# Kernel optimization log

Measured on AMD Instinct MI355X. Metric: run time of the kernel, lower is better.

## Reference

```python
import jax, jax.numpy as jnp
import numpy as np

N_HEADS = 8
EMBED_DIM = 512
HEAD_DIM = EMBED_DIM // N_HEADS
INPUT_DIM = 512


def setup_inputs() -> dict:
    key = jax.random.key(0)
    ks = jax.random.split(key, 9)
    B, N = 4, 2048
    s_in = 1.0 / np.sqrt(INPUT_DIM)
    s_e = 1.0 / np.sqrt(EMBED_DIM)
    return {
        "q": jax.random.normal(ks[0], (B, N, INPUT_DIM), dtype=jnp.float32),
        "wq": jax.random.uniform(ks[1], (EMBED_DIM, INPUT_DIM), jnp.float32, -s_in, s_in),
        "bq": jax.random.uniform(ks[2], (EMBED_DIM,), jnp.float32, -s_in, s_in),
        "wk": jax.random.uniform(ks[3], (EMBED_DIM, INPUT_DIM), jnp.float32, -s_in, s_in),
        "bk": jax.random.uniform(ks[4], (EMBED_DIM,), jnp.float32, -s_in, s_in),
        "wv": jax.random.uniform(ks[5], (EMBED_DIM, INPUT_DIM), jnp.float32, -s_in, s_in),
        "bv": jax.random.uniform(ks[6], (EMBED_DIM,), jnp.float32, -s_in, s_in),
        "wo": jax.random.uniform(ks[7], (EMBED_DIM, EMBED_DIM), jnp.float32, -s_e, s_e),
        "bo": jax.random.uniform(ks[8], (EMBED_DIM,), jnp.float32, -s_e, s_e),
    }


def reference(q, wq, bq, wk, bk, wv, bv, wo, bo):
    B, N, _ = q.shape
    # linear projections (torch Linear: x @ W.T + b)
    Q = (q @ wq.T + bq).reshape(B, N, N_HEADS, HEAD_DIM).transpose(0, 2, 1, 3)
    K = (q @ wk.T + bk).reshape(B, N, N_HEADS, HEAD_DIM).transpose(0, 2, 1, 3)
    V = (q @ wv.T + bv).reshape(B, N, N_HEADS, HEAD_DIM).transpose(0, 2, 1, 3)
    scores = jnp.einsum("bhqd,bhkd->bhqk", Q, K) / jnp.sqrt(
        jnp.asarray(HEAD_DIM, dtype=q.dtype)
    )
    weights = jax.nn.softmax(scores, axis=-1)
    out = jnp.einsum("bhqk,bhkd->bhqd", weights, V)  # [B,H,N,Dh]
    out = out.transpose(0, 2, 1, 3).reshape(B, N, EMBED_DIM)
    return out @ wo.T + bo
```

## Files before the change

### kernel.cpp

```cpp
#include <hip/hip_runtime.h>
#include <hip/hip_bf16.h>
#include <math.h>

#define SEQ    2048
#define DH     64
#define EMB    512
#define INDIM  512
#define NHEADS 8
#define BATCH  4
#define MTOT   (BATCH * SEQ)

typedef __attribute__((ext_vector_type(8))) short bf16x8;
typedef __attribute__((ext_vector_type(4))) float f32x4;

__device__ __forceinline__ ushort f2bf(float x) {
  union { float f; unsigned u; } v; v.f = x;
  unsigned r = v.u + 0x7FFFu + ((v.u >> 16) & 1u);
  return (ushort)(r >> 16);
}

__device__ __forceinline__ unsigned cvt_pk_bf16(float lo, float hi) {
  unsigned r;
  asm("v_cvt_pk_bf16_f32 %0, %1, %2" : "=v"(r) : "v"(lo), "v"(hi));
  return r;
}

__device__ __forceinline__ float fast_exp2(float x) {
  float r;
  asm("v_exp_f32 %0, %1" : "=v"(r) : "v"(x));
  return r;
}

__device__ __forceinline__ void permswap32(unsigned &x, unsigned &y) {
  asm("v_permlane32_swap_b32 %0, %1" : "+v"(x), "+v"(y));
}

__global__ __launch_bounds__(256) void conv_bf16(const float* __restrict__ src,
                                                 ushort* __restrict__ dst, int n8) {
  const int i = blockIdx.x * 256 + threadIdx.x;
  if (i >= n8) return;
  const float4 a = ((const float4*)src)[i * 2];
  const float4 b = ((const float4*)src)[i * 2 + 1];
  uint4 o;
  o.x = cvt_pk_bf16(a.x, a.y);
  o.y = cvt_pk_bf16(a.z, a.w);
  o.z = cvt_pk_bf16(b.x, b.y);
  o.w = cvt_pk_bf16(b.z, b.w);
  ((uint4*)dst)[i] = o;
}

__global__ __launch_bounds__(256) void conv_bf16_w4(
    const float* __restrict__ w0, const float* __restrict__ w1,
    const float* __restrict__ w2, const float* __restrict__ w3,
    ushort* __restrict__ dst, int n8per) {
  const int i = blockIdx.x * 256 + threadIdx.x;
  if (i >= n8per) return;
  const float* src = (blockIdx.y == 0) ? w0 : (blockIdx.y == 1) ? w1
                   : (blockIdx.y == 2) ? w2 : w3;
  ushort* d = dst + (size_t)blockIdx.y * n8per * 8;
  const float4 a = ((const float4*)src)[i * 2];
  const float4 b = ((const float4*)src)[i * 2 + 1];
  uint4 o;
  o.x = cvt_pk_bf16(a.x, a.y);
  o.y = cvt_pk_bf16(a.z, a.w);
  o.z = cvt_pk_bf16(b.x, b.y);
  o.w = cvt_pk_bf16(b.z, b.w);
  ((uint4*)d)[i] = o;
}

template <int MODE>
__global__ __launch_bounds__(256) void mfma_gemm(
    const ushort* __restrict__ A, const ushort* __restrict__ W,
    const float* __restrict__ b0, const float* __restrict__ b1,
    const float* __restrict__ b2,
    ushort* __restrict__ outQ, ushort* __restrict__ outK,
    ushort* __restrict__ outVT, float* __restrict__ outF) {
  __shared__ __align__(16) char smem[MODE == 0 ? 35840 : 16384];
  ushort* As = (ushort*)smem;
  ushort* Bs = (ushort*)(smem + 8192);
  ushort* Tl = (ushort*)smem;
  ushort* Tl2 = (ushort*)smem;

  const int bm = blockIdx.x * 128;
  const int bn = blockIdx.y * 128;
  const int tid = threadIdx.x;
  const int wave = tid >> 6, lane = tid & 63;
  const int g = lane >> 4, ln = lane & 15;
  const int wr = wave >> 1, wc = wave & 1;

  f32x4 acc[4][4];
#pragma unroll
  for (int m = 0; m < 4; ++m)
#pragma unroll
    for (int n = 0; n < 4; ++n) acc[m][n] = (f32x4){0.f, 0.f, 0.f, 0.f};

  const size_t a_base = (size_t)(bm + wave * 16 + (lane >> 2)) * INDIM + (lane & 3) * 8;
  const size_t b_base = (size_t)(bn + wave * 16 + (lane >> 2)) * INDIM + (lane & 3) * 8;
  ushort* ldsA0 = As + wave * 512;
  ushort* ldsA1 = As + 2048 + wave * 512;
  ushort* ldsB0 = Bs + wave * 512;
  ushort* ldsB1 = Bs + 2048 + wave * 512;

  for (int k0 = 0; k0 < INDIM; k0 += 32) {
    __syncthreads();
    __builtin_amdgcn_global_load_lds(
        (const __attribute__((address_space(1))) void*)(A + a_base + k0),
        (__attribute__((address_space(3))) void*)ldsA0, 16, 0, 0);
    __builtin_amdgcn_global_load_lds(
        (const __attribute__((address_space(1))) void*)(A + a_base + 64 * INDIM + k0),
        (__attribute__((address_space(3))) void*)ldsA1, 16, 0, 0);
    __builtin_amdgcn_global_load_lds(
        (const __attribute__((address_space(1))) void*)(W + b_base + k0),
        (__attribute__((address_space(3))) void*)ldsB0, 16, 0, 0);
    __builtin_amdgcn_global_load_lds(
        (const __attribute__((address_space(1))) void*)(W + b_base + 64 * INDIM + k0),
        (__attribute__((address_space(3))) void*)ldsB1, 16, 0, 0);
    __syncthreads();

    bf16x8 af[4], bfv[4];
#pragma unroll
    for (int m = 0; m < 4; ++m)
      af[m] = *(const bf16x8*)&As[(64 * wr + 16 * m + ln) * 32 + 8 * g];
#pragma unroll
    for (int n = 0; n < 4; ++n)
      bfv[n] = *(const bf16x8*)&Bs[(64 * wc + 16 * n + ln) * 32 + 8 * g];
#pragma unroll
    for (int m = 0; m < 4; ++m)
#pragma unroll
      for (int n = 0; n < 4; ++n)
        acc[m][n] = __builtin_amdgcn_mfma_f32_16x16x32_bf16(af[m], bfv[n], acc[m][n], 0, 0, 0);
  }

  if (MODE == 1) {
#pragma unroll
    for (int n = 0; n < 4; ++n) {
      const int e = bn + 64 * wc + 16 * n + ln;
      const float bv = b0[e];
#pragma unroll
      for (int m = 0; m < 4; ++m)
#pragma unroll
        for (int r = 0; r < 4; ++r) {
          const int row = bm + 64 * wr + 16 * m + 4 * g + r;
          outF[(size_t)row * EMB + e] = acc[m][n][r] + bv;
        }
    }
    return;
  }

  const int which = bn >> 9;
  const float* bias = (which == 0) ? b0 : (which == 1) ? b1 : b2;

  if (which < 2) {
    const float scl = (which == 0) ? 0.18033688f : 1.0f;
    ushort* dst = (which == 0) ? outQ : outK;
    __syncthreads();
#pragma unroll
    for (int n = 0; n < 4; ++n) {
      const int cl = 64 * wc + 16 * n + ln;
      const float bv = bias[(bn & 511) + cl];
#pragma unroll
      for (int m = 0; m < 4; ++m)
#pragma unroll
        for (int r = 0; r < 4; ++r) {
          const int rl = 64 * wr + 16 * m + 4 * g + r;
          Tl2[rl * 136 + cl] = f2bf((acc[m][n][r] + bv) * scl);
        }
    }
    __syncthreads();
#pragma unroll
    for (int j = 0; j < 8; ++j) {
      const int cid = j * 256 + tid;
      const int seg = cid >> 3;
      const int l8 = cid & 7;
      const int rl = seg >> 1, half = seg & 1;
      const int row = bm + rl;
      const int b = row >> 11, nn = row & (SEQ - 1);
      const int h = ((bn & 511) >> 6) + half;
      const bf16x8 v = *(const bf16x8*)&Tl2[rl * 136 + half * 64 + l8 * 8];
      *(bf16x8*)&dst[(((size_t)(b * NHEADS + h) * SEQ) + nn) * DH + l8 * 8] = v;
    }
  } else {
    __syncthreads();
#pragma unroll
    for (int n = 0; n < 4; ++n) {
      const int cl = 64 * wc + 16 * n + ln;
      const float bv = bias[(bn & 511) + cl];
#pragma unroll
      for (int m = 0; m < 4; ++m)
#pragma unroll
        for (int r = 0; r < 4; ++r) {
          const int rl = 64 * wr + 16 * m + 4 * g + r;
          Tl[cl * 140 + rl] = f2bf(acc[m][n][r] + bv);
        }
    }
    __syncthreads();
    const int c = tid >> 1;
    const int rh = (tid & 1) * 64;
    const int e = (bn & 511) + c;
    const int h = e >> 6, d = e & 63;
    const int b = bm >> 11;
    const int nn0 = (bm & (SEQ - 1)) + rh;
    ushort* drow = outVT + (((size_t)(b * NHEADS + h) * DH) + d) * SEQ + nn0;
#pragma unroll
    for (int j = 0; j < 8; ++j)
      *(bf16x8*)&drow[j * 8] = *(const bf16x8*)&Tl[c * 140 + rh + j * 8];
  }
}

__global__ __launch_bounds__(256, 4) void attn_mfma(const ushort* __restrict__ Q,
                                                    const ushort* __restrict__ K,
                                                    const ushort* __restrict__ VT,
                                                    ushort* __restrict__ O) {
  __shared__ __align__(16) ushort Kl[2][64 * 72];
  __shared__ __align__(16) ushort Vl[2][64 * 72];

  const int tid = threadIdx.x;
  const int wave = tid >> 6, lane = tid & 63;
  const int g = lane >> 4, ln = lane & 15;

  const int orig = blockIdx.x;
  const int swz = (orig & 7) * 128 + (orig >> 3);
  const int bh = swz >> 5;
  const int qx = swz & 31;
  const int qbase = qx * 64 + wave * 16;

  const ushort* Qb = Q + ((size_t)bh * SEQ + qbase) * DH;
  const ushort* Kb = K + (size_t)bh * SEQ * DH;
  const ushort* Vb = VT + (size_t)bh * DH * SEQ;

  const bf16x8 qf0 = *(const bf16x8*)&Qb[ln * DH + 8 * g];
  const bf16x8 qf1 = *(const bf16x8*)&Qb[ln * DH + 32 + 8 * g];

  bf16x8 vones;
#pragma unroll
  for (int i = 0; i < 8; ++i) vones[i] = (short)0x3F80;

  f32x4 oacc[4];
  f32x4 oaccD = (f32x4){0.f, 0.f, 0.f, 0.f};
#pragma unroll
  for (int t = 0; t < 4; ++t) oacc[t] = (f32x4){0.f, 0.f, 0.f, 0.f};

  const int skv = tid >> 3, sd = (tid & 7) * 8;
  const int dt = tid >> 2, kc = (tid & 3) * 8;
  const int pr0 = skv ^ (((((skv >> 2) ^ (skv >> 3)) & 1)) * 12);
  const int s32 = skv + 32;
  const int pr1 = s32 ^ (((((s32 >> 2) ^ (s32 >> 3)) & 1)) * 12);

  bf16x8 k0v = *(const bf16x8*)&Kb[(size_t)skv * DH + sd];
  bf16x8 k1v = *(const bf16x8*)&Kb[(size_t)(32 + skv) * DH + sd];
  bf16x8 v0v = *(const bf16x8*)&Vb[(size_t)dt * SEQ + kc];
  bf16x8 v1v = *(const bf16x8*)&Vb[(size_t)dt * SEQ + 32 + kc];
  *(bf16x8*)&Kl[0][pr0 * 72 + sd] = k0v;
  *(bf16x8*)&Kl[0][pr1 * 72 + sd] = k1v;
  *(bf16x8*)&Vl[0][dt * 72 + kc] = v0v;
  *(bf16x8*)&Vl[0][dt * 72 + 32 + kc] = v1v;
  k0v = *(const bf16x8*)&Kb[(size_t)(64 + skv) * DH + sd];
  k1v = *(const bf16x8*)&Kb[(size_t)(96 + skv) * DH + sd];
  v0v = *(const bf16x8*)&Vb[(size_t)dt * SEQ + 64 + kc];
  v1v = *(const bf16x8*)&Vb[(size_t)dt * SEQ + 96 + kc];
  asm volatile("s_waitcnt lgkmcnt(0)" ::: "memory");
  __builtin_amdgcn_s_barrier();

  for (int it = 0; it < 32; ++it) {
    const int cur = it & 1;
    ushort* Kc = Kl[cur];
    ushort* Vc = Vl[cur];

    if (it < 31) {
      ushort* Kn = Kl[cur ^ 1];
      ushort* Vn = Vl[cur ^ 1];
      *(bf16x8*)&Kn[pr0 * 72 + sd] = k0v;
      *(bf16x8*)&Kn[pr1 * 72 + sd] = k1v;
      *(bf16x8*)&Vn[dt * 72 + kc] = v0v;
      *(bf16x8*)&Vn[dt * 72 + 32 + kc] = v1v;
    }
    {
      const int nxt = (it + 2 < 32) ? (it + 2) * 64 : 31 * 64;
      k0v = *(const bf16x8*)&Kb[(size_t)(nxt + skv) * DH + sd];
      k1v = *(const bf16x8*)&Kb[(size_t)(nxt + 32 + skv) * DH + sd];
      v0v = *(const bf16x8*)&Vb[(size_t)dt * SEQ + nxt + kc];
      v1v = *(const bf16x8*)&Vb[(size_t)dt * SEQ + nxt + 32 + kc];
    }

    bf16x8 ka[4][2], vb[2][4];
#pragma unroll
    for (int t = 0; t < 4; ++t) {
      ka[t][0] = *(const bf16x8*)&Kc[(16 * t + ln) * 72 + 8 * g];
      ka[t][1] = *(const bf16x8*)&Kc[(16 * t + ln) * 72 + 32 + 8 * g];
    }
#pragma unroll
    for (int c = 0; c < 2; ++c)
#pragma unroll
      for (int t = 0; t < 4; ++t)
        vb[c][t] = *(const bf16x8*)&Vc[(16 * t + ln) * 72 + 32 * c + 8 * g];

    f32x4 s0 = (f32x4){0.f, 0.f, 0.f, 0.f};
    f32x4 s1 = s0, s2 = s0, s3 = s0;
    __builtin_amdgcn_s_setprio(1);
    s0 = __builtin_amdgcn_mfma_f32_16x16x32_bf16(ka[0][0], qf0, s0, 0, 0, 0);
    s1 = __builtin_amdgcn_mfma_f32_16x16x32_bf16(ka[1][0], qf0, s1, 0, 0, 0);
    s2 = __builtin_amdgcn_mfma_f32_16x16x32_bf16(ka[2][0], qf0, s2, 0, 0, 0);
    s3 = __builtin_amdgcn_mfma_f32_16x16x32_bf16(ka[3][0], qf0, s3, 0, 0, 0);
    s0 = __builtin_amdgcn_mfma_f32_16x16x32_bf16(ka[0][1], qf1, s0, 0, 0, 0);
    s1 = __builtin_amdgcn_mfma_f32_16x16x32_bf16(ka[1][1], qf1, s1, 0, 0, 0);
    s2 = __builtin_amdgcn_mfma_f32_16x16x32_bf16(ka[2][1], qf1, s2, 0, 0, 0);
    s3 = __builtin_amdgcn_mfma_f32_16x16x32_bf16(ka[3][1], qf1, s3, 0, 0, 0);
    __builtin_amdgcn_s_setprio(0);

    float p0[4], p1[4], p2[4], p3[4];
#pragma unroll
    for (int r = 0; r < 4; ++r) {
      p0[r] = fast_exp2(s0[r]);
      p1[r] = fast_exp2(s1[r]);
      p2[r] = fast_exp2(s2[r]);
      p3[r] = fast_exp2(s3[r]);
    }

    unsigned a0 = cvt_pk_bf16(p0[0], p0[1]);
    unsigned a2 = cvt_pk_bf16(p1[0], p1[1]);
    unsigned a1 = cvt_pk_bf16(p0[2], p0[3]);
    unsigned a3 = cvt_pk_bf16(p1[2], p1[3]);
    permswap32(a0, a2);
    permswap32(a1, a3);
    unsigned b0 = cvt_pk_bf16(p2[0], p2[1]);
    unsigned b2 = cvt_pk_bf16(p3[0], p3[1]);
    unsigned b1 = cvt_pk_bf16(p2[2], p2[3]);
    unsigned b3 = cvt_pk_bf16(p3[2], p3[3]);
    permswap32(b0, b2);
    permswap32(b1, b3);
    union { unsigned u[4]; bf16x8 v; } pa0, pa1;
    pa0.u[0] = a0; pa0.u[1] = a1; pa0.u[2] = a2; pa0.u[3] = a3;
    pa1.u[0] = b0; pa1.u[1] = b1; pa1.u[2] = b2; pa1.u[3] = b3;

    __builtin_amdgcn_s_setprio(1);
#pragma unroll
    for (int t = 0; t < 4; ++t) {
      oacc[t] = __builtin_amdgcn_mfma_f32_16x16x32_bf16(pa0.v, vb[0][t], oacc[t], 0, 0, 0);
      oacc[t] = __builtin_amdgcn_mfma_f32_16x16x32_bf16(pa1.v, vb[1][t], oacc[t], 0, 0, 0);
    }
    oaccD = __builtin_amdgcn_mfma_f32_16x16x32_bf16(pa0.v, vones, oaccD, 0, 0, 0);
    oaccD = __builtin_amdgcn_mfma_f32_16x16x32_bf16(pa1.v, vones, oaccD, 0, 0, 0);
    __builtin_amdgcn_s_setprio(0);

    asm volatile("s_waitcnt lgkmcnt(0)" ::: "memory");
    __builtin_amdgcn_s_barrier();
  }

  const int b = bh >> 3, h = bh & 7;
#pragma unroll
  for (int r = 0; r < 4; ++r) {
    const float ir = 1.0f / oaccD[r];
    ushort* op = O + ((size_t)(b * SEQ) + qbase + 4 * g + r) * EMB + h * 64;
#pragma unroll
    for (int t = 0; t < 4; ++t) op[16 * t + ln] = f2bf(oacc[t][r] * ir);
  }
}

extern "C" void kernel_launch(void* const* d_in, const int* in_sizes, int n_in,
                              void* d_out, int out_size, void* d_ws, size_t ws_size,
                              hipStream_t stream) {
  const float* q  = (const float*)d_in[0];
  const float* wq = (const float*)d_in[1];
  const float* bq = (const float*)d_in[2];
  const float* wk = (const float*)d_in[3];
  const float* bk = (const float*)d_in[4];
  const float* wv = (const float*)d_in[5];
  const float* bv = (const float*)d_in[6];
  const float* wo = (const float*)d_in[7];
  const float* bo = (const float*)d_in[8];
  float* out = (float*)d_out;

  const size_t XSZ = (size_t)MTOT * INDIM;
  const size_t WSZ = (size_t)EMB * INDIM;
  const size_t QSZ = (size_t)BATCH * NHEADS * SEQ * DH;
  ushort* wsX = (ushort*)d_ws;
  ushort* wsW = wsX + XSZ;
  ushort* wsQ = wsW + 4 * WSZ;
  ushort* wsK = wsQ + QSZ;
  ushort* wsVT = wsK + QSZ;
  ushort* wsA = wsVT + QSZ;

  const dim3 blk(256);

  conv_bf16<<<dim3(XSZ / 8 / 256), blk, 0, stream>>>(q, wsX, XSZ / 8);
  conv_bf16_w4<<<dim3(WSZ / 8 / 256, 4), blk, 0, stream>>>(wq, wk, wv, wo, wsW, WSZ / 8);

  mfma_gemm<0><<<dim3(MTOT / 128, 1536 / 128), blk, 0, stream>>>(
      wsX, wsW, bq, bk, bv, wsQ, wsK, wsVT, nullptr);

  attn_mfma<<<dim3(1024), blk, 0, stream>>>(wsQ, wsK, wsVT, wsA);

  mfma_gemm<1><<<dim3(MTOT / 128, EMB / 128), blk, 0, stream>>>(
      wsA, wsW + 3 * WSZ, bo, nullptr, nullptr, nullptr, nullptr, nullptr, out);
}
```

Measured before the change: 106.7 us.

## Process two 16-row query tiles per wave in attention to reuse K/V fragments

Each wave in the attention kernel now handles 32 query rows (two 16-row MFMA tiles) instead of 16, so each block covers 128 queries and the grid is halved to 512 blocks. The K and V fragments read from LDS are reused across both query tiles, and the QK and PV MFMAs for the two tiles are interleaved. The aim is to halve LDS traffic and global K/V loads per unit of work. In exchange, register pressure roughly doubles (the occupancy hint in launch bounds is dropped) and fewer blocks are available to fill the device.

```diff
diff --git a/kernel.cpp b/kernel.cpp
--- a/kernel.cpp
+++ b/kernel.cpp
@@ -207,10 +207,10 @@
   }
 }
 
-__global__ __launch_bounds__(256, 4) void attn_mfma(const ushort* __restrict__ Q,
-                                                    const ushort* __restrict__ K,
-                                                    const ushort* __restrict__ VT,
-                                                    ushort* __restrict__ O) {
+__global__ __launch_bounds__(256) void attn_mfma(const ushort* __restrict__ Q,
+                                                 const ushort* __restrict__ K,
+                                                 const ushort* __restrict__ VT,
+                                                 ushort* __restrict__ O) {
   __shared__ __align__(16) ushort Kl[2][64 * 72];
   __shared__ __align__(16) ushort Vl[2][64 * 72];
 
@@ -219,26 +219,32 @@
   const int g = lane >> 4, ln = lane & 15;
 
   const int orig = blockIdx.x;
-  const int swz = (orig & 7) * 128 + (orig >> 3);
-  const int bh = swz >> 5;
-  const int qx = swz & 31;
-  const int qbase = qx * 64 + wave * 16;
+  const int swz = (orig & 7) * 64 + (orig >> 3);
+  const int bh = swz >> 4;
+  const int qx = swz & 15;
+  const int qbase = qx * 128 + wave * 32;
 
   const ushort* Qb = Q + ((size_t)bh * SEQ + qbase) * DH;
   const ushort* Kb = K + (size_t)bh * SEQ * DH;
   const ushort* Vb = VT + (size_t)bh * DH * SEQ;
 
-  const bf16x8 qf0 = *(const bf16x8*)&Qb[ln * DH + 8 * g];
-  const bf16x8 qf1 = *(const bf16x8*)&Qb[ln * DH + 32 + 8 * g];
+  const bf16x8 qfA0 = *(const bf16x8*)&Qb[ln * DH + 8 * g];
+  const bf16x8 qfA1 = *(const bf16x8*)&Qb[ln * DH + 32 + 8 * g];
+  const bf16x8 qfB0 = *(const bf16x8*)&Qb[(16 + ln) * DH + 8 * g];
+  const bf16x8 qfB1 = *(const bf16x8*)&Qb[(16 + ln) * DH + 32 + 8 * g];
 
   bf16x8 vones;
 #pragma unroll
   for (int i = 0; i < 8; ++i) vones[i] = (short)0x3F80;
 
-  f32x4 oacc[4];
-  f32x4 oaccD = (f32x4){0.f, 0.f, 0.f, 0.f};
-#pragma unroll
-  for (int t = 0; t < 4; ++t) oacc[t] = (f32x4){0.f, 0.f, 0.f, 0.f};
+  f32x4 oaccA[4], oaccB[4];
+  f32x4 oaccDA = (f32x4){0.f, 0.f, 0.f, 0.f};
+  f32x4 oaccDB = (f32x4){0.f, 0.f, 0.f, 0.f};
+#pragma unroll
+  for (int t = 0; t < 4; ++t) {
+    oaccA[t] = (f32x4){0.f, 0.f, 0.f, 0.f};
+    oaccB[t] = (f32x4){0.f, 0.f, 0.f, 0.f};
+  }
 
   const int skv = tid >> 3, sd = (tid & 7) * 8;
   const int dt = tid >> 2, kc = (tid & 3) * 8;
@@ -294,52 +300,84 @@
       for (int t = 0; t < 4; ++t)
         vb[c][t] = *(const bf16x8*)&Vc[(16 * t + ln) * 72 + 32 * c + 8 * g];
 
-    f32x4 s0 = (f32x4){0.f, 0.f, 0.f, 0.f};
-    f32x4 s1 = s0, s2 = s0, s3 = s0;
+    f32x4 sA0 = (f32x4){0.f, 0.f, 0.f, 0.f};
+    f32x4 sA1 = sA0, sA2 = sA0, sA3 = sA0;
+    f32x4 sB0 = sA0, sB1 = sA0, sB2 = sA0, sB3 = sA0;
     __builtin_amdgcn_s_setprio(1);
-    s0 = __builtin_amdgcn_mfma_f32_16x16x32_bf16(ka[0][0], qf0, s0, 0, 0, 0);
-    s1 = __builtin_amdgcn_mfma_f32_16x16x32_bf16(ka[1][0], qf0, s1, 0, 0, 0);
-    s2 = __builtin_amdgcn_mfma_f32_16x16x32_bf16(ka[2][0], qf0, s2, 0, 0, 0);
-    s3 = __builtin_amdgcn_mfma_f32_16x16x32_bf16(ka[3][0], qf0, s3, 0, 0, 0);
-    s0 = __builtin_amdgcn_mfma_f32_16x16x32_bf16(ka[0][1], qf1, s0, 0, 0, 0);
-    s1 = __builtin_amdgcn_mfma_f32_16x16x32_bf16(ka[1][1], qf1, s1, 0, 0, 0);
-    s2 = __builtin_amdgcn_mfma_f32_16x16x32_bf16(ka[2][1], qf1, s2, 0, 0, 0);
-    s3 = __builtin_amdgcn_mfma_f32_16x16x32_bf16(ka[3][1], qf1, s3, 0, 0, 0);
+    sA0 = __builtin_amdgcn_mfma_f32_16x16x32_bf16(ka[0][0], qfA0, sA0, 0, 0, 0);
+    sB0 = __builtin_amdgcn_mfma_f32_16x16x32_bf16(ka[0][0], qfB0, sB0, 0, 0, 0);
+    sA1 = __builtin_amdgcn_mfma_f32_16x16x32_bf16(ka[1][0], qfA0, sA1, 0, 0, 0);
+    sB1 = __builtin_amdgcn_mfma_f32_16x16x32_bf16(ka[1][0], qfB0, sB1, 0, 0, 0);
+    sA2 = __builtin_amdgcn_mfma_f32_16x16x32_bf16(ka[2][0], qfA0, sA2, 0, 0, 0);
+    sB2 = __builtin_amdgcn_mfma_f32_16x16x32_bf16(ka[2][0], qfB0, sB2, 0, 0, 0);
+    sA3 = __builtin_amdgcn_mfma_f32_16x16x32_bf16(ka[3][0], qfA0, sA3, 0, 0, 0);
+    sB3 = __builtin_amdgcn_mfma_f32_16x16x32_bf16(ka[3][0], qfB0, sB3, 0, 0, 0);
+    sA0 = __builtin_amdgcn_mfma_f32_16x16x32_bf16(ka[0][1], qfA1, sA0, 0, 0, 0);
+    sB0 = __builtin_amdgcn_mfma_f32_16x16x32_bf16(ka[0][1], qfB1, sB0, 0, 0, 0);
+    sA1 = __builtin_amdgcn_mfma_f32_16x16x32_bf16(ka[1][1], qfA1, sA1, 0, 0, 0);
+    sB1 = __builtin_amdgcn_mfma_f32_16x16x32_bf16(ka[1][1], qfB1, sB1, 0, 0, 0);
+    sA2 = __builtin_amdgcn_mfma_f32_16x16x32_bf16(ka[2][1], qfA1, sA2, 0, 0, 0);
+    sB2 = __builtin_amdgcn_mfma_f32_16x16x32_bf16(ka[2][1], qfB1, sB2, 0, 0, 0);
+    sA3 = __builtin_amdgcn_mfma_f32_16x16x32_bf16(ka[3][1], qfA1, sA3, 0, 0, 0);
+    sB3 = __builtin_amdgcn_mfma_f32_16x16x32_bf16(ka[3][1], qfB1, sB3, 0, 0, 0);
     __builtin_amdgcn_s_setprio(0);
 
-    float p0[4], p1[4], p2[4], p3[4];
+    float pA0[4], pA1[4], pA2[4], pA3[4];
+    float pB0[4], pB1[4], pB2[4], pB3[4];
 #pragma unroll
     for (int r = 0; r < 4; ++r) {
-      p0[r] = fast_exp2(s0[r]);
-      p1[r] = fast_exp2(s1[r]);
-      p2[r] = fast_exp2(s2[r]);
-      p3[r] = fast_exp2(s3[r]);
-    }
-
-    unsigned a0 = cvt_pk_bf16(p0[0], p0[1]);
-    unsigned a2 = cvt_pk_bf16(p1[0], p1[1]);
-    unsigned a1 = cvt_pk_bf16(p0[2], p0[3]);
-    unsigned a3 = cvt_pk_bf16(p1[2], p1[3]);
-    permswap32(a0, a2);
-    permswap32(a1, a3);
-    unsigned b0 = cvt_pk_bf16(p2[0], p2[1]);
-    unsigned b2 = cvt_pk_bf16(p3[0], p3[1]);
-    unsigned b1 = cvt_pk_bf16(p2[2], p2[3]);
-    unsigned b3 = cvt_pk_bf16(p3[2], p3[3]);
-    permswap32(b0, b2);
-    permswap32(b1, b3);
-    union { unsigned u[4]; bf16x8 v; } pa0, pa1;
-    pa0.u[0] = a0; pa0.u[1] = a1; pa0.u[2] = a2; pa0.u[3] = a3;
-    pa1.u[0] = b0; pa1.u[1] = b1; pa1.u[2] = b2; pa1.u[3] = b3;
+      pA0[r] = fast_exp2(sA0[r]);
+      pA1[r] = fast_exp2(sA1[r]);
+      pA2[r] = fast_exp2(sA2[r]);
+      pA3[r] = fast_exp2(sA3[r]);
+      pB0[r] = fast_exp2(sB0[r]);
+      pB1[r] = fast_exp2(sB1[r]);
+      pB2[r] = fast_exp2(sB2[r]);
+      pB3[r] = fast_exp2(sB3[r]);
+    }
+
+    unsigned aa0 = cvt_pk_bf16(pA0[0], pA0[1]);
+    unsigned aa2 = cvt_pk_bf16(pA1[0], pA1[1]);
+    unsigned aa1 = cvt_pk_bf16(pA0[2], pA0[3]);
+    unsigned aa3 = cvt_pk_bf16(pA1[2], pA1[3]);
+    permswap32(aa0, aa2);
+    permswap32(aa1, aa3);
+    unsigned ab0 = cvt_pk_bf16(pA2[0], pA2[1]);
+    unsigned ab2 = cvt_pk_bf16(pA3[0], pA3[1]);
+    unsigned ab1 = cvt_pk_bf16(pA2[2], pA2[3]);
+    unsigned ab3 = cvt_pk_bf16(pA3[2], pA3[3]);
+    permswap32(ab0, ab2);
+    permswap32(ab1, ab3);
+    unsigned ba0 = cvt_pk_bf16(pB0[0], pB0[1]);
+    unsigned ba2 = cvt_pk_bf16(pB1[0], pB1[1]);
+    unsigned ba1 = cvt_pk_bf16(pB0[2], pB0[3]);
+    unsigned ba3 = cvt_pk_bf16(pB1[2], pB1[3]);
+    permswap32(ba0, ba2);
+    permswap32(ba1, ba3);
+    unsigned bb0 = cvt_pk_bf16(pB2[0], pB2[1]);
+    unsigned bb2 = cvt_pk_bf16(pB3[0], pB3[1]);
+    unsigned bb1 = cvt_pk_bf16(pB2[2], pB2[3]);
+    unsigned bb3 = cvt_pk_bf16(pB3[2], pB3[3]);
+    permswap32(bb0, bb2);
+    permswap32(bb1, bb3);
+    union { unsigned u[4]; bf16x8 v; } paA0, paA1, paB0, paB1;
+    paA0.u[0] = aa0; paA0.u[1] = aa1; paA0.u[2] = aa2; paA0.u[3] = aa3;
+    paA1.u[0] = ab0; paA1.u[1] = ab1; paA1.u[2] = ab2; paA1.u[3] = ab3;
+    paB0.u[0] = ba0; paB0.u[1] = ba1; paB0.u[2] = ba2; paB0.u[3] = ba3;
+    paB1.u[0] = bb0; paB1.u[1] = bb1; paB1.u[2] = bb2; paB1.u[3] = bb3;
 
     __builtin_amdgcn_s_setprio(1);
 #pragma unroll
     for (int t = 0; t < 4; ++t) {
-      oacc[t] = __builtin_amdgcn_mfma_f32_16x16x32_bf16(pa0.v, vb[0][t], oacc[t], 0, 0, 0);
-      oacc[t] = __builtin_amdgcn_mfma_f32_16x16x32_bf16(pa1.v, vb[1][t], oacc[t], 0, 0, 0);
-    }
-    oaccD = __builtin_amdgcn_mfma_f32_16x16x32_bf16(pa0.v, vones, oaccD, 0, 0, 0);
-    oaccD = __builtin_amdgcn_mfma_f32_16x16x32_bf16(pa1.v, vones, oaccD, 0, 0, 0);
+      oaccA[t] = __builtin_amdgcn_mfma_f32_16x16x32_bf16(paA0.v, vb[0][t], oaccA[t], 0, 0, 0);
+      oaccB[t] = __builtin_amdgcn_mfma_f32_16x16x32_bf16(paB0.v, vb[0][t], oaccB[t], 0, 0, 0);
+      oaccA[t] = __builtin_amdgcn_mfma_f32_16x16x32_bf16(paA1.v, vb[1][t], oaccA[t], 0, 0, 0);
+      oaccB[t] = __builtin_amdgcn_mfma_f32_16x16x32_bf16(paB1.v, vb[1][t], oaccB[t], 0, 0, 0);
+    }
+    oaccDA = __builtin_amdgcn_mfma_f32_16x16x32_bf16(paA0.v, vones, oaccDA, 0, 0, 0);
+    oaccDB = __builtin_amdgcn_mfma_f32_16x16x32_bf16(paB0.v, vones, oaccDB, 0, 0, 0);
+    oaccDA = __builtin_amdgcn_mfma_f32_16x16x32_bf16(paA1.v, vones, oaccDA, 0, 0, 0);
+    oaccDB = __builtin_amdgcn_mfma_f32_16x16x32_bf16(paB1.v, vones, oaccDB, 0, 0, 0);
     __builtin_amdgcn_s_setprio(0);
 
     asm volatile("s_waitcnt lgkmcnt(0)" ::: "memory");
@@ -349,10 +387,15 @@
   const int b = bh >> 3, h = bh & 7;
 #pragma unroll
   for (int r = 0; r < 4; ++r) {
-    const float ir = 1.0f / oaccD[r];
-    ushort* op = O + ((size_t)(b * SEQ) + qbase + 4 * g + r) * EMB + h * 64;
-#pragma unroll
-    for (int t = 0; t < 4; ++t) op[16 * t + ln] = f2bf(oacc[t][r] * ir);
+    const float irA = 1.0f / oaccDA[r];
+    const float irB = 1.0f / oaccDB[r];
+    ushort* opA = O + ((size_t)(b * SEQ) + qbase + 4 * g + r) * EMB + h * 64;
+    ushort* opB = O + ((size_t)(b * SEQ) + qbase + 16 + 4 * g + r) * EMB + h * 64;
+#pragma unroll
+    for (int t = 0; t < 4; ++t) {
+      opA[16 * t + ln] = f2bf(oaccA[t][r] * irA);
+      opB[16 * t + ln] = f2bf(oaccB[t][r] * irB);
+    }
   }
 }
 
@@ -388,7 +431,7 @@
   mfma_gemm<0><<<dim3(MTOT / 128, 1536 / 128), blk, 0, stream>>>(
       wsX, wsW, bq, bk, bv, wsQ, wsK, wsVT, nullptr);
 
-  attn_mfma<<<dim3(1024), blk, 0, stream>>>(wsQ, wsK, wsVT, wsA);
+  attn_mfma<<<dim3(512), blk, 0, stream>>>(wsQ, wsK, wsVT, wsA);
 
   mfma_gemm<1><<<dim3(MTOT / 128, EMB / 128), blk, 0, stream>>>(
       wsA, wsW + 3 * WSZ, bo, nullptr, nullptr, nullptr, nullptr, nullptr, out);
```

After: 100.9 us. 1.06x faster.
